# Kernel tuning notes

Measured on AMD Instinct MI355X. Metric: run time of the kernel, lower is better.

Reference implementation:

```python
import jax, jax.numpy as jnp
import numpy as np

N_NODES = 50000
N_EDGES = 400000
DIMS = [128, 256, 512, 256, 64, 2]


def setup_inputs() -> dict:
    key = jax.random.key(0)
    ks = jax.random.split(key, 16)
    x = jax.random.normal(ks[0], (N_NODES, DIMS[0]), dtype=jnp.float32)
    edge_index = jax.random.randint(ks[1], (2, N_EDGES), 0, N_NODES, dtype=jnp.int64)
    inp = {"x": x, "edge_index": edge_index}
    for i in range(5):
        fan_in, fan_out = DIMS[i], DIMS[i + 1]
        scale = (2.0 / (fan_in + fan_out)) ** 0.5  # glorot-ish
        inp[f"W{i+1}"] = jax.random.normal(ks[2 + 2 * i], (fan_in, fan_out), dtype=jnp.float32) * scale
        inp[f"b{i+1}"] = jnp.zeros((fan_out,), dtype=jnp.float32)
    return inp


def _gcn_norm(edge_index, n):
    # add self-loops, compute symmetric normalization D^{-1/2} A_hat D^{-1/2}
    loop = jnp.arange(n, dtype=edge_index.dtype)
    src = jnp.concatenate([edge_index[0], loop])
    dst = jnp.concatenate([edge_index[1], loop])
    deg = jax.ops.segment_sum(jnp.ones_like(dst, dtype=jnp.float32), dst, num_segments=n)
    dinv = jnp.where(deg > 0, jax.lax.rsqrt(deg), 0.0)
    norm = dinv[src] * dinv[dst]  # [E+N]
    return src, dst, norm


def _gcn_conv(h, W, b, src, dst, norm, n):
    h = h @ W                                   # [N, out]
    msg = h[src] * norm[:, None]                # gather + scale, [E+N, out]
    out = jax.ops.segment_sum(msg, dst, num_segments=n)  # scatter-add
    return out + b


def reference(x, edge_index, W1, b1, W2, b2, W3, b3, W4, b4, W5, b5):
    n = x.shape[0]
    src, dst, norm = _gcn_norm(edge_index, n)
    h = jax.nn.relu(_gcn_conv(x, W1, b1, src, dst, norm, n))
    h = jax.nn.relu(_gcn_conv(h, W2, b2, src, dst, norm, n))
    h = jax.nn.relu(_gcn_conv(h, W3, b3, src, dst, norm, n))
    h = jax.nn.relu(_gcn_conv(h, W4, b4, src, dst, norm, n))
    h = _gcn_conv(h, W5, b5, src, dst, norm, n)
    return jax.nn.log_softmax(h, axis=1)
```

## Files before the change

kernel.cpp:

```cpp
#include <hip/hip_runtime.h>
#include <math.h>

#define N_NODES 50000
#define N_EDGES 400000

typedef __bf16 bf16x8 __attribute__((ext_vector_type(8)));
typedef float f32x4 __attribute__((ext_vector_type(4)));

__device__ __forceinline__ unsigned bf16_rne(float v) {
    unsigned u = __float_as_uint(v);
    return (u + 0x7FFFu + ((u >> 16) & 1u)) >> 16;
}
__device__ __forceinline__ unsigned pack_split(float v) {
    unsigned hi = bf16_rne(v);
    float hif = __uint_as_float(hi << 16);
    unsigned lo = bf16_rne(v - hif);
    return (hi << 16) | lo;
}
__device__ __forceinline__ float unpack_ps(unsigned w) {
    return __uint_as_float(w & 0xFFFF0000u) + __uint_as_float(w << 16);
}

__global__ void k_zero_i(int* __restrict__ p, int n) {
    int i = blockIdx.x * blockDim.x + threadIdx.x;
    if (i < n) p[i] = 0;
}

__global__ void k_count(const int* __restrict__ dst, int* __restrict__ cnt) {
    int e = blockIdx.x * blockDim.x + threadIdx.x;
    if (e < N_EDGES) atomicAdd(&cnt[dst[e]], 1);
}

__global__ __launch_bounds__(1024) void k_scan(const int* __restrict__ cnt,
                                               int* __restrict__ rowptr,
                                               float* __restrict__ dinv, int n) {
    __shared__ int sm[1024];
    __shared__ int carry;
    if (threadIdx.x == 0) carry = 0;
    __syncthreads();
    for (int base = 0; base < n; base += 1024) {
        int i = base + threadIdx.x;
        int v = (i < n) ? cnt[i] : 0;
        sm[threadIdx.x] = v;
        __syncthreads();
        for (int off = 1; off < 1024; off <<= 1) {
            int t = (threadIdx.x >= (unsigned)off) ? sm[threadIdx.x - off] : 0;
            __syncthreads();
            sm[threadIdx.x] += t;
            __syncthreads();
        }
        if (i < n) {
            rowptr[i] = carry + sm[threadIdx.x] - v;
            dinv[i] = rsqrtf((float)(v + 1));
        }
        __syncthreads();
        if (threadIdx.x == 0) carry += sm[1023];
        __syncthreads();
    }
    if (threadIdx.x == 0) rowptr[n] = carry;
}

__global__ void k_copy_i(const int* __restrict__ s, int* __restrict__ d, int n) {
    int i = blockIdx.x * blockDim.x + threadIdx.x;
    if (i < n) d[i] = s[i];
}

__global__ void k_fill(const int* __restrict__ src, const int* __restrict__ dst,
                       int* __restrict__ cursor, int* __restrict__ csr) {
    int e = blockIdx.x * blockDim.x + threadIdx.x;
    if (e >= N_EDGES) return;
    int d = dst[e];
    int pos = atomicAdd(&cursor[d], 1);
    csr[pos] = src[e];
}

__global__ void k_wprep(const float* __restrict__ W, unsigned* __restrict__ Wtp, int K, int N) {
    int i = blockIdx.x * blockDim.x + threadIdx.x;
    if (i >= K * N) return;
    int k = i / N, n = i % N;
    Wtp[(size_t)n * K + k] = pack_split(W[i]);
}

__global__ void k_rowscale(const float* __restrict__ x, const float* __restrict__ dinv,
                           float* __restrict__ xs) {
    int idx = blockIdx.x * blockDim.x + threadIdx.x;
    if (idx >= N_NODES * 32) return;
    int i = idx >> 5;
    float4 v = ((const float4*)x)[idx];
    float s = dinv[i];
    v.x *= s; v.y *= s; v.z *= s; v.w *= s;
    ((float4*)xs)[idx] = v;
}

template <int VEC, int MODE, int INP, int OUTP>
__global__ __launch_bounds__(256) void k_agg(
    const void* __restrict__ gv, const int* __restrict__ rowptr,
    const int* __restrict__ csr, const float* __restrict__ dinv,
    const float* __restrict__ bias, void* __restrict__ ov)
{
    constexpr int W = 64 * VEC;
    const int wave = threadIdx.x >> 6, lane = threadIdx.x & 63;
    const int node = blockIdx.x * 4 + wave;
    if (node >= N_NODES) return;
    const int col = lane * VEC;

    float acc[VEC];
#pragma unroll
    for (int v = 0; v < VEC; ++v) acc[v] = 0.f;

    auto fetch_add = [&](int r) {
        if constexpr (INP) {
            const unsigned* p = (const unsigned*)gv + (size_t)r * W + col;
            if constexpr (VEC == 4) {
                uint4 t = *(const uint4*)p;
                acc[0] += unpack_ps(t.x); acc[1] += unpack_ps(t.y);
                acc[2] += unpack_ps(t.z); acc[3] += unpack_ps(t.w);
            } else if constexpr (VEC == 2) {
                uint2 t = *(const uint2*)p;
                acc[0] += unpack_ps(t.x); acc[1] += unpack_ps(t.y);
            } else acc[0] += unpack_ps(*p);
        } else {
            const float* p = (const float*)gv + (size_t)r * W + col;
            if constexpr (VEC == 4) {
                float4 t = *(const float4*)p;
                acc[0] += t.x; acc[1] += t.y; acc[2] += t.z; acc[3] += t.w;
            } else if constexpr (VEC == 2) {
                float2 t = *(const float2*)p;
                acc[0] += t.x; acc[1] += t.y;
            } else acc[0] += *(const float*)p;
        }
    };

    fetch_add(node);
    const int beg = rowptr[node], end = rowptr[node + 1];
    for (int j = beg; j < end; ++j) fetch_add(csr[j]);

    const float sc = dinv[node];
    float r[VEC];
#pragma unroll
    for (int v = 0; v < VEC; ++v) {
        float t = sc * acc[v];
        if (MODE == 1) t = fmaxf(t + bias[col + v], 0.f);
        r[v] = t;
    }
    if constexpr (OUTP) {
        unsigned* po = (unsigned*)ov + (size_t)node * W + col;
        if constexpr (VEC == 4)
            *(uint4*)po = make_uint4(pack_split(r[0]), pack_split(r[1]), pack_split(r[2]), pack_split(r[3]));
        else if constexpr (VEC == 2)
            *(uint2*)po = make_uint2(pack_split(r[0]), pack_split(r[1]));
        else *po = pack_split(r[0]);
    } else {
        float* po = (float*)ov + (size_t)node * W + col;
        if constexpr (VEC == 4) *(float4*)po = make_float4(r[0], r[1], r[2], r[3]);
        else if constexpr (VEC == 2) *(float2*)po = make_float2(r[0], r[1]);
        else *po = r[0];
    }
}

__global__ void k_agg2(const float* __restrict__ g, const int* __restrict__ rowptr,
                       const int* __restrict__ csr, const float* __restrict__ dinv,
                       float* __restrict__ o) {
    int i = blockIdx.x * blockDim.x + threadIdx.x;
    if (i >= N_NODES) return;
    float2 a = *(const float2*)&g[2 * (size_t)i];
    int beg = rowptr[i], end = rowptr[i + 1];
    for (int j = beg; j < end; ++j) {
        int s = csr[j];
        float2 t = *(const float2*)&g[2 * (size_t)s];
        a.x += t.x; a.y += t.y;
    }
    float sc = dinv[i];
    o[2 * (size_t)i + 0] = sc * a.x;
    o[2 * (size_t)i + 1] = sc * a.y;
}

template <int WM, int WN>
__global__ __launch_bounds__(256) void k_gemm_mfma(
    const unsigned* __restrict__ Ap, const unsigned* __restrict__ Wtp,
    const float* __restrict__ dinv, const float* __restrict__ bias,
    unsigned* __restrict__ Gp, int M, int K, int N, int mode)
{
    constexpr int BM = 2 * WM, BN = 2 * WN;
    constexpr int AF = WM / 16, BF = WN / 16;
    constexpr int ACH = BM / 32, BCH = BN / 32;
    constexpr int BUF = (2 * BM + 2 * BN) * 64;
    __shared__ char lds[2 * BUF];

    const int tid = threadIdx.x;
    const int m0 = blockIdx.y * BM;
    const int n0 = blockIdx.x * BN;
    const int wv = tid >> 6, l = tid & 63;
    const int wr = wv >> 1, wc = wv & 1;
    const int lr = l & 15, ls = l >> 4;

    int aoff[AF], boff[BF];
#pragma unroll
    for (int f = 0; f < AF; ++f) {
        int row = wr * WM + f * 16 + lr;
        aoff[f] = (row * 64 + ls * 16) ^ ((row & 7) << 4);
    }
#pragma unroll
    for (int j = 0; j < BF; ++j) {
        int row = wc * WN + j * 16 + lr;
        boff[j] = (row * 64 + ls * 16) ^ ((row & 7) << 4);
    }

    uint4 ra[ACH], rb[BCH];

    auto issue = [&](int kt) {
#pragma unroll
        for (int p = 0; p < ACH; ++p) {
            int c = p * 256 + tid;
            int row = c >> 3, c4 = (c & 7) << 2;
            int grow = m0 + row;
            ra[p] = make_uint4(0u, 0u, 0u, 0u);
            if (grow < M) ra[p] = *(const uint4*)&Ap[(size_t)grow * K + kt + c4];
        }
#pragma unroll
        for (int p = 0; p < BCH; ++p) {
            int c = p * 256 + tid;
            int row = c >> 3, c4 = (c & 7) << 2;
            rb[p] = *(const uint4*)&Wtp[(size_t)(n0 + row) * K + kt + c4];
        }
    };

    auto commit = [&](int buf) {
        char* Ahi = lds + buf * BUF;
        char* Alo = Ahi + BM * 64;
        char* Bhi = Alo + BM * 64;
        char* Blo = Bhi + BN * 64;
#pragma unroll
        for (int p = 0; p < ACH; ++p) {
            int c = p * 256 + tid;
            int row = c >> 3, c4 = (c & 7) << 2;
            uint4 w = ra[p];
            ushort4 hi, lo;
            hi.x = w.x >> 16; lo.x = w.x & 0xFFFFu;
            hi.y = w.y >> 16; lo.y = w.y & 0xFFFFu;
            hi.z = w.z >> 16; lo.z = w.z & 0xFFFFu;
            hi.w = w.w >> 16; lo.w = w.w & 0xFFFFu;
            int off = (row * 64 + c4 * 2) ^ ((row & 7) << 4);
            *(ushort4*)(Ahi + off) = hi;
            *(ushort4*)(Alo + off) = lo;
        }
#pragma unroll
        for (int p = 0; p < BCH; ++p) {
            int c = p * 256 + tid;
            int row = c >> 3, c4 = (c & 7) << 2;
            uint4 w = rb[p];
            ushort4 hi, lo;
            hi.x = w.x >> 16; lo.x = w.x & 0xFFFFu;
            hi.y = w.y >> 16; lo.y = w.y & 0xFFFFu;
            hi.z = w.z >> 16; lo.z = w.z & 0xFFFFu;
            hi.w = w.w >> 16; lo.w = w.w & 0xFFFFu;
            int off = (row * 64 + c4 * 2) ^ ((row & 7) << 4);
            *(ushort4*)(Bhi + off) = hi;
            *(ushort4*)(Blo + off) = lo;
        }
    };

    f32x4 acc[AF][BF] = {};
    const int nt = K / 32;

    issue(0);
    commit(0);
    __syncthreads();
    int cur = 0;

    for (int t = 0; t < nt; ++t) {
        if (t + 1 < nt) issue((t + 1) * 32);

        const char* base = lds + cur * BUF;
        bf16x8 ah[AF], al[AF], bh[BF], bl[BF];
#pragma unroll
        for (int f = 0; f < AF; ++f) {
            ah[f] = *(const bf16x8*)(base + aoff[f]);
            al[f] = *(const bf16x8*)(base + BM * 64 + aoff[f]);
        }
#pragma unroll
        for (int j = 0; j < BF; ++j) {
            bh[j] = *(const bf16x8*)(base + 2 * BM * 64 + boff[j]);
            bl[j] = *(const bf16x8*)(base + 2 * BM * 64 + BN * 64 + boff[j]);
        }
#pragma unroll
        for (int f = 0; f < AF; ++f)
#pragma unroll
            for (int j = 0; j < BF; ++j) {
                acc[f][j] = __builtin_amdgcn_mfma_f32_16x16x32_bf16(ah[f], bh[j], acc[f][j], 0, 0, 0);
                acc[f][j] = __builtin_amdgcn_mfma_f32_16x16x32_bf16(ah[f], bl[j], acc[f][j], 0, 0, 0);
                acc[f][j] = __builtin_amdgcn_mfma_f32_16x16x32_bf16(al[f], bh[j], acc[f][j], 0, 0, 0);
            }

        if (t + 1 < nt) {
            commit(cur ^ 1);
            __syncthreads();
            cur ^= 1;
        }
    }

#pragma unroll
    for (int f = 0; f < AF; ++f)
#pragma unroll
        for (int j = 0; j < BF; ++j) {
            int col = n0 + wc * WN + j * 16 + lr;
            float bc = (mode >= 1) ? bias[col] : 0.f;
#pragma unroll
            for (int reg = 0; reg < 4; ++reg) {
                int r = m0 + wr * WM + f * 16 + ls * 4 + reg;
                if (r < M) {
                    float t = acc[f][j][reg];
                    if (mode == 0)      t = dinv[r] * t;
                    else if (mode == 1) t = fmaxf(t + bc, 0.f);
                    else                t = dinv[r] * fmaxf(t + bc, 0.f);
                    Gp[(size_t)r * N + col] = pack_split(t);
                }
            }
        }
}

__global__ void k_gemm2(const float* __restrict__ A, const float* __restrict__ W,
                        const float* __restrict__ dinv, float* __restrict__ G, int M, int K)
{
    int i = blockIdx.x * blockDim.x + threadIdx.x;
    if (i >= M) return;
    float a0 = 0.f, a1 = 0.f;
    for (int k = 0; k < K; k += 4) {
        float4 a = *(const float4*)&A[(size_t)i * K + k];
        a0 += a.x * W[(k + 0) * 2 + 0] + a.y * W[(k + 1) * 2 + 0]
            + a.z * W[(k + 2) * 2 + 0] + a.w * W[(k + 3) * 2 + 0];
        a1 += a.x * W[(k + 0) * 2 + 1] + a.y * W[(k + 1) * 2 + 1]
            + a.z * W[(k + 2) * 2 + 1] + a.w * W[(k + 3) * 2 + 1];
    }
    float s = dinv[i];
    G[2 * (size_t)i + 0] = s * a0;
    G[2 * (size_t)i + 1] = s * a1;
}

__global__ void k_final(const float* __restrict__ lg, const float* __restrict__ bias,
                        float* __restrict__ out, int M)
{
    int i = blockIdx.x * blockDim.x + threadIdx.x;
    if (i >= M) return;
    float o0 = lg[2 * (size_t)i + 0] + bias[0];
    float o1 = lg[2 * (size_t)i + 1] + bias[1];
    float m = fmaxf(o0, o1);
    float lse = m + logf(expf(o0 - m) + expf(o1 - m));
    out[2 * (size_t)i + 0] = o0 - lse;
    out[2 * (size_t)i + 1] = o1 - lse;
}

extern "C" void kernel_launch(void* const* d_in, const int* in_sizes, int n_in,
                              void* d_out, int out_size, void* d_ws, size_t ws_size,
                              hipStream_t stream) {
    const float* x   = (const float*)d_in[0];
    const int*   ei  = (const int*)d_in[1];
    const int*   src = ei;
    const int*   dst = ei + N_EDGES;
    const float* W1 = (const float*)d_in[2];  const float* b1 = (const float*)d_in[3];
    const float* W2 = (const float*)d_in[4];  const float* b2 = (const float*)d_in[5];
    const float* W3 = (const float*)d_in[6];  const float* b3 = (const float*)d_in[7];
    const float* W4 = (const float*)d_in[8];  const float* b4 = (const float*)d_in[9];
    const float* W5 = (const float*)d_in[10]; const float* b5 = (const float*)d_in[11];
    float* out = (float*)d_out;

    char* ws = (char*)d_ws;
    float*    dinv   = (float*)(ws + 0);
    int*      cnt    = (int*)(ws + 256 * 1024);
    int*      rowptr = (int*)(ws + 512 * 1024);
    int*      cursor = (int*)(ws + 768 * 1024);
    int*      csr    = (int*)(ws + 1024 * 1024);
    unsigned* wt1 = (unsigned*)(ws + 3 * 1024 * 1024);
    unsigned* wt2 = wt1 + 128 * 256;
    unsigned* wt3 = wt2 + 256 * 512;
    unsigned* wt4 = wt3 + 512 * 256;

    char* D = ws + 6 * 1024 * 1024;
    float*    xs   = (float*)D;
    unsigned* aggx = (unsigned*)(D + (size_t)N_NODES * 128 * 4);
    unsigned* h1s  = (unsigned*)(D + (size_t)N_NODES * 512 * 4);
    unsigned* a2   = (unsigned*)(D + (size_t)N_NODES * 768 * 4);
    unsigned* h2   = (unsigned*)D;
    unsigned* g3s  = h1s;
    unsigned* h3   = a2;
    unsigned* g4s  = (unsigned*)D;
    float*    h4   = (float*)(D + (size_t)N_NODES * 64 * 4);
    float*    g5s  = (float*)(D + (size_t)N_NODES * 128 * 4);
    float*    lgt  = (float*)(D + (size_t)N_NODES * 132 * 4);

    const int T = 256;
    const int nodeB = (N_NODES + T - 1) / T;
    const int edgeB = (N_EDGES + T - 1) / T;
    const int aggB  = (N_NODES + 3) / 4;
    const int gy    = (N_NODES + 63) / 64;

    k_zero_i<<<nodeB, T, 0, stream>>>(cnt, N_NODES);
    k_count<<<edgeB, T, 0, stream>>>(dst, cnt);
    k_scan<<<1, 1024, 0, stream>>>(cnt, rowptr, dinv, N_NODES);
    k_copy_i<<<nodeB, T, 0, stream>>>(rowptr, cursor, N_NODES);
    k_fill<<<edgeB, T, 0, stream>>>(src, dst, cursor, csr);
    k_wprep<<<(128 * 256 + T - 1) / T, T, 0, stream>>>(W1, wt1, 128, 256);
    k_wprep<<<(256 * 512 + T - 1) / T, T, 0, stream>>>(W2, wt2, 256, 512);
    k_wprep<<<(512 * 256 + T - 1) / T, T, 0, stream>>>(W3, wt3, 512, 256);
    k_wprep<<<(256 * 64 + T - 1) / T, T, 0, stream>>>(W4, wt4, 256, 64);

    k_rowscale<<<(N_NODES * 32 + T - 1) / T, T, 0, stream>>>(x, dinv, xs);
    k_agg<2, 0, 0, 1><<<aggB, T, 0, stream>>>(xs, rowptr, csr, dinv, nullptr, aggx);
    k_gemm_mfma<32, 64><<<dim3(2, gy), T, 0, stream>>>(aggx, wt1, dinv, b1, h1s, N_NODES, 128, 256, 2);

    k_agg<4, 0, 1, 1><<<aggB, T, 0, stream>>>(h1s, rowptr, csr, dinv, nullptr, a2);
    k_gemm_mfma<32, 64><<<dim3(4, gy), T, 0, stream>>>(a2, wt2, dinv, b2, h2, N_NODES, 256, 512, 1);

    k_gemm_mfma<32, 64><<<dim3(2, gy), T, 0, stream>>>(h2, wt3, dinv, nullptr, g3s, N_NODES, 512, 256, 0);
    k_agg<4, 1, 1, 1><<<aggB, T, 0, stream>>>(g3s, rowptr, csr, dinv, b3, h3);

    k_gemm_mfma<32, 32><<<dim3(1, gy), T, 0, stream>>>(h3, wt4, dinv, nullptr, g4s, N_NODES, 256, 64, 0);
    k_agg<1, 1, 1, 0><<<aggB, T, 0, stream>>>(g4s, rowptr, csr, dinv, b4, h4);

    k_gemm2<<<nodeB, T, 0, stream>>>(h4, W5, dinv, g5s, N_NODES, 64);
    k_agg2<<<nodeB, T, 0, stream>>>(g5s, rowptr, csr, dinv, lgt);
    k_final<<<nodeB, T, 0, stream>>>(lgt, b5, out, N_NODES);
}
```

Baseline: 704.3 us.

## Replace single-block serial prefix scan with three-phase multi-block scan

```diff
diff --git a/kernel.cpp b/kernel.cpp
--- a/kernel.cpp
+++ b/kernel.cpp
@@ -31,38 +31,53 @@
     if (e < N_EDGES) atomicAdd(&cnt[dst[e]], 1);
 }
 
-__global__ __launch_bounds__(1024) void k_scan(const int* __restrict__ cnt,
-                                               int* __restrict__ rowptr,
-                                               float* __restrict__ dinv, int n) {
+__global__ __launch_bounds__(1024) void k_scan1(const int* __restrict__ cnt,
+                                                int* __restrict__ loc,
+                                                int* __restrict__ part, int n) {
     __shared__ int sm[1024];
-    __shared__ int carry;
-    if (threadIdx.x == 0) carry = 0;
+    const int tid = threadIdx.x;
+    const int i = blockIdx.x * 1024 + tid;
+    int v = (i < n) ? cnt[i] : 0;
+    sm[tid] = v;
     __syncthreads();
-    for (int base = 0; base < n; base += 1024) {
-        int i = base + threadIdx.x;
-        int v = (i < n) ? cnt[i] : 0;
-        sm[threadIdx.x] = v;
+    for (int off = 1; off < 1024; off <<= 1) {
+        int t = (tid >= off) ? sm[tid - off] : 0;
         __syncthreads();
-        for (int off = 1; off < 1024; off <<= 1) {
-            int t = (threadIdx.x >= (unsigned)off) ? sm[threadIdx.x - off] : 0;
-            __syncthreads();
-            sm[threadIdx.x] += t;
-            __syncthreads();
-        }
-        if (i < n) {
-            rowptr[i] = carry + sm[threadIdx.x] - v;
-            dinv[i] = rsqrtf((float)(v + 1));
-        }
+        sm[tid] += t;
         __syncthreads();
-        if (threadIdx.x == 0) carry += sm[1023];
+    }
+    if (i < n) loc[i] = sm[tid] - v;
+    if (tid == 1023) part[blockIdx.x] = sm[1023];
+}
+
+__global__ void k_scan2(int* __restrict__ part, int* __restrict__ total, int nb) {
+    __shared__ int sm[64];
+    const int tid = threadIdx.x;
+    int v = (tid < nb) ? part[tid] : 0;
+    sm[tid] = v;
+    __syncthreads();
+    for (int off = 1; off < 64; off <<= 1) {
+        int t = (tid >= off) ? sm[tid - off] : 0;
         __syncthreads();
-    }
-    if (threadIdx.x == 0) rowptr[n] = carry;
-}
-
-__global__ void k_copy_i(const int* __restrict__ s, int* __restrict__ d, int n) {
-    int i = blockIdx.x * blockDim.x + threadIdx.x;
-    if (i < n) d[i] = s[i];
+        sm[tid] += t;
+        __syncthreads();
+    }
+    if (tid < nb) part[tid] = sm[tid] - v;
+    if (tid == 63) *total = sm[63];
+}
+
+__global__ void k_scan3(const int* __restrict__ cnt, const int* __restrict__ loc,
+                        const int* __restrict__ part, const int* __restrict__ total,
+                        int* __restrict__ rowptr, int* __restrict__ cursor,
+                        float* __restrict__ dinv, int n) {
+    int i = blockIdx.x * blockDim.x + threadIdx.x;
+    if (i < n) {
+        int r = loc[i] + part[i >> 10];
+        rowptr[i] = r;
+        cursor[i] = r;
+        dinv[i] = rsqrtf((float)(cnt[i] + 1));
+    }
+    if (i == 0) rowptr[n] = *total;
 }
 
 __global__ void k_fill(const int* __restrict__ src, const int* __restrict__ dst,
@@ -370,10 +385,13 @@
     int*      rowptr = (int*)(ws + 512 * 1024);
     int*      cursor = (int*)(ws + 768 * 1024);
     int*      csr    = (int*)(ws + 1024 * 1024);
+    int*      part   = (int*)(ws + 2700 * 1024);
+    int*      total  = (int*)(ws + 2702 * 1024);
     unsigned* wt1 = (unsigned*)(ws + 3 * 1024 * 1024);
     unsigned* wt2 = wt1 + 128 * 256;
     unsigned* wt3 = wt2 + 256 * 512;
     unsigned* wt4 = wt3 + 512 * 256;
+    int*      loc    = (int*)(ws + 5 * 1024 * 1024);
 
     char* D = ws + 6 * 1024 * 1024;
     float*    xs   = (float*)D;
@@ -393,11 +411,13 @@
     const int edgeB = (N_EDGES + T - 1) / T;
     const int aggB  = (N_NODES + 3) / 4;
     const int gy    = (N_NODES + 63) / 64;
+    const int scanB = (N_NODES + 1023) / 1024;
 
     k_zero_i<<<nodeB, T, 0, stream>>>(cnt, N_NODES);
     k_count<<<edgeB, T, 0, stream>>>(dst, cnt);
-    k_scan<<<1, 1024, 0, stream>>>(cnt, rowptr, dinv, N_NODES);
-    k_copy_i<<<nodeB, T, 0, stream>>>(rowptr, cursor, N_NODES);
+    k_scan1<<<scanB, 1024, 0, stream>>>(cnt, loc, part, N_NODES);
+    k_scan2<<<1, 64, 0, stream>>>(part, total, scanB);
+    k_scan3<<<nodeB, T, 0, stream>>>(cnt, loc, part, total, rowptr, cursor, dinv, N_NODES);
     k_fill<<<edgeB, T, 0, stream>>>(src, dst, cursor, csr);
     k_wprep<<<(128 * 256 + T - 1) / T, T, 0, stream>>>(W1, wt1, 128, 256);
     k_wprep<<<(256 * 512 + T - 1) / T, T, 0, stream>>>(W2, wt2, 256, 512);
```

Result: faster. 620.8 us (-11.9%).
